# Kernel optimization log

Measured on AMD Instinct MI355X. Metric: run time of the kernel, lower is better.

## Reference

```python
import jax, jax.numpy as jnp
import numpy as np


def setup_inputs() -> dict:
    key = jax.random.key(0)
    ks = jax.random.split(key, 6)
    dim, dt_rank, dim_inner, d_state, channels, batch = 1024, 64, 1024, 128, 64, 8
    rn = lambda k, shape, sc: (jax.random.normal(k, shape, jnp.float32) * sc)
    return {
        "x": rn(ks[0], (batch, channels, dim), 1.0),
        "proj_w": rn(ks[1], (dim, dim), dim ** -0.5),
        "proj_b": jnp.zeros((dim,), jnp.float32),
        "conv_w": rn(ks[2], (channels, channels, 3), (channels * 3) ** -0.5),
        "conv_b": jnp.zeros((channels,), jnp.float32),
        "deltaBC_w": rn(ks[3], (dt_rank + 2 * d_state, dim), dim ** -0.5),
        "dt_proj_w": rn(ks[4], (dim_inner, dt_rank), dt_rank ** -0.5),
        "dt_proj_b": jnp.zeros((dim_inner,), jnp.float32),
        "A_log": jnp.log(jnp.broadcast_to(
            jnp.arange(1, d_state + 1, dtype=jnp.float32), (dim_inner, d_state))),
        "D": jnp.ones((dim_inner,), jnp.float32),
    }


def _silu(x):
    return x * jax.nn.sigmoid(x)


def _selective_scan(x, delta, A, B, C, D):
    # x, delta: (b, l, ed); A: (ed, n); B, C: (b, l, n); D: (ed)
    deltaA = jnp.exp(delta[..., None] * A)                      # (b, l, ed, n)
    BX = delta[..., None] * B[:, :, None, :] * x[..., None]     # (b, l, ed, n)

    def binop(e1, e2):
        a1, b1 = e1
        a2, b2 = e2
        return a1 * a2, a2 * b1 + b2

    # h_t = deltaA_t * h_{t-1} + BX_t  (parallel scan over sequence axis)
    _, hs = jax.lax.associative_scan(binop, (deltaA, BX), axis=1)
    y = jnp.einsum("blen,bln->ble", hs, C) + D * x
    return y


def reference(x, proj_w, proj_b, conv_w, conv_b, deltaBC_w,
              dt_proj_w, dt_proj_b, A_log, D):
    dt_rank = dt_proj_w.shape[1]
    d_state = A_log.shape[1]

    skip = x
    # same self.proj applied to both branches
    x1 = x @ proj_w.T + proj_b
    x2 = x1

    # Conv1d over the feature axis, treating seq positions as channels (L == channels)
    x1 = jax.lax.conv_general_dilated(
        x1, conv_w, window_strides=(1,), padding=[(1, 1)],
        dimension_numbers=("NCH", "OIH", "NCH")) + conv_b[None, :, None]
    x1 = _silu(x1)

    # SSM
    A = -jnp.exp(A_log)
    dbc = x1 @ deltaBC_w.T                                      # (b, l, dt_rank + 2n)
    delta = dbc[..., :dt_rank]
    Bm = dbc[..., dt_rank:dt_rank + d_state]
    Cm = dbc[..., dt_rank + d_state:]
    delta = jax.nn.softplus(delta @ dt_proj_w.T + dt_proj_b)    # (b, l, ed)
    y = _selective_scan(x1, delta, A, Bm, Cm, D)

    out = y * _silu(x2) + skip
    return out @ proj_w.T + proj_b
```

## Files before the change

kernel.cpp:

```cpp
#include <hip/hip_runtime.h>
#include <hip/hip_bf16.h>
#include <math.h>

typedef __hip_bfloat16 bf16;
typedef __attribute__((ext_vector_type(8))) short bf16x8;
typedef __attribute__((ext_vector_type(4))) float f32x4;

#define DIM     1024
#define DT_RANK 64
#define D_STATE 128
#define CHAN    64
#define BATCH   8
#define ROWS    (BATCH*CHAN)
#define DBC_N   (DT_RANK + 2*D_STATE)

#define SZ_X    (ROWS*DIM)
#define SZ_PW   (DIM*DIM)
#define SZ_PB   (DIM)
#define SZ_CW   (CHAN*CHAN*3)
#define SZ_CB   (CHAN)
#define SZ_DBCW (DBC_N*DIM)
#define SZ_DTW  (DIM*DT_RANK)
#define SZ_DTB  (DIM)
#define SZ_ALOG (DIM*D_STATE)
#define SZ_D    (DIM)

#define O0 0
#define O1 (O0+SZ_X)
#define O2 (O1+SZ_PW)
#define O3 (O2+SZ_PB)
#define O4 (O3+SZ_CW)
#define O5 (O4+SZ_CB)
#define O6 (O5+SZ_DBCW)
#define O7 (O6+SZ_DTW)
#define O8 (O7+SZ_DTB)
#define O9 (O8+SZ_ALOG)
#define TOTAL (O9+SZ_D)

#define BF16_ONES_PAIR 0x3F803F80u

__device__ __forceinline__ unsigned short f2b(float v) {
    bf16 t = __float2bfloat16(v);
    return *reinterpret_cast<unsigned short*>(&t);
}
__device__ __forceinline__ float b162f(unsigned short s) {
    return __uint_as_float(((unsigned)s) << 16);
}
__device__ __forceinline__ const bf16* SELP(const void* din, const bf16* wsp, int isb) {
    return isb ? (const bf16*)din : wsp;
}

__global__ __launch_bounds__(256) void convert_kernel(
    const void* __restrict__ s0, const void* __restrict__ s1,
    const void* __restrict__ s2, const void* __restrict__ s3,
    const void* __restrict__ s4, const void* __restrict__ s5,
    const void* __restrict__ s6, const void* __restrict__ s7,
    const void* __restrict__ s8, const void* __restrict__ s9,
    bf16* __restrict__ dstb)
{
    if (*(const unsigned*)s9 == BF16_ONES_PAIR) return;
    int idx = (blockIdx.x * 256 + threadIdx.x) * 4;
    if (idx >= TOTAL) return;
    const void* src; int base;
    if      (idx < O1) { src = s0; base = O0; }
    else if (idx < O2) { src = s1; base = O1; }
    else if (idx < O3) { src = s2; base = O2; }
    else if (idx < O4) { src = s3; base = O3; }
    else if (idx < O5) { src = s4; base = O4; }
    else if (idx < O6) { src = s5; base = O5; }
    else if (idx < O7) { src = s6; base = O6; }
    else if (idx < O8) { src = s7; base = O7; }
    else if (idx < O9) { src = s8; base = O8; }
    else               { src = s9; base = O9; }
    const int rel = idx - base;
    float4 v = *reinterpret_cast<const float4*>((const float*)src + rel);
    ushort4 u; u.x = f2b(v.x); u.y = f2b(v.y); u.z = f2b(v.z); u.w = f2b(v.w);
    *reinterpret_cast<ushort4*>(&dstb[idx]) = u;
}

template<int ACT, int OUTMODE, int K>
__global__ __launch_bounds__(256) void gemm_mfma(
    const void* __restrict__ Ad, const bf16* __restrict__ Aw,
    const void* __restrict__ Bd, const bf16* __restrict__ Bw,
    const void* __restrict__ biasd, const bf16* __restrict__ biasw,
    void* __restrict__ C0, bf16* __restrict__ C1,
    int lda, int ldb, int ldc, const unsigned* __restrict__ dsrc)
{
    __shared__ float red[4][32][36];
    const int isb = (*dsrc == BF16_ONES_PAIR) ? 1 : 0;
    const bf16* A = SELP(Ad, Aw, isb);
    const bf16* B = SELP(Bd, Bw, isb);
    const bf16* bias = (Ad == nullptr && Aw == nullptr) ? nullptr : nullptr;
    const bf16* biasp = (biasd || biasw) ? SELP(biasd, biasw, isb) : nullptr;

    const int l  = threadIdx.x & 63;
    const int w  = threadIdx.x >> 6;
    const int m0 = blockIdx.y * 32;
    const int n0 = blockIdx.x * 32;
    const int fr = l & 15;
    const int ko = (l >> 4) * 8;
    (void)bias;

    const bf16* Abase = A + (size_t)(m0 + fr) * lda + ko;
    const bf16* Bbase = B + (size_t)(n0 + fr) * ldb + ko;

    f32x4 acc00 = {}, acc01 = {}, acc10 = {}, acc11 = {};

    #pragma unroll 4
    for (int ks = w; ks * 32 < K; ks += 4) {
        const int k0 = ks * 32;
        bf16x8 a0 = *reinterpret_cast<const bf16x8*>(Abase + k0);
        bf16x8 a1 = *reinterpret_cast<const bf16x8*>(Abase + (size_t)16 * lda + k0);
        bf16x8 b0 = *reinterpret_cast<const bf16x8*>(Bbase + k0);
        bf16x8 b1 = *reinterpret_cast<const bf16x8*>(Bbase + (size_t)16 * ldb + k0);
        acc00 = __builtin_amdgcn_mfma_f32_16x16x32_bf16(a0, b0, acc00, 0, 0, 0);
        acc01 = __builtin_amdgcn_mfma_f32_16x16x32_bf16(a0, b1, acc01, 0, 0, 0);
        acc10 = __builtin_amdgcn_mfma_f32_16x16x32_bf16(a1, b0, acc10, 0, 0, 0);
        acc11 = __builtin_amdgcn_mfma_f32_16x16x32_bf16(a1, b1, acc11, 0, 0, 0);
    }

    {
        const int cr = (l >> 4) * 4;
        const int cc = l & 15;
        #pragma unroll
        for (int v = 0; v < 4; ++v) {
            red[w][cr + v][cc]           = acc00[v];
            red[w][cr + v][16 + cc]      = acc01[v];
            red[w][16 + cr + v][cc]      = acc10[v];
            red[w][16 + cr + v][16 + cc] = acc11[v];
        }
    }
    __syncthreads();

    const int t = threadIdx.x;
    const int r = t >> 3;
    const int c = (t & 7) * 4;
    float o[4];
    #pragma unroll
    for (int q = 0; q < 4; ++q) {
        float s = red[0][r][c + q] + red[1][r][c + q]
                + red[2][r][c + q] + red[3][r][c + q];
        if (biasp) s += __bfloat162float(biasp[n0 + c + q]);
        if (ACT == 1) s = (s > 20.0f) ? s : log1pf(__expf(s));
        o[q] = s;
    }
    const int m = m0 + r, nn = n0 + c;
    const size_t off = (size_t)m * ldc + nn;
    if (OUTMODE == 0) {
        *reinterpret_cast<float4*>((float*)C0 + off) = make_float4(o[0], o[1], o[2], o[3]);
    } else if (OUTMODE == 3) {
        ushort4 u; u.x = f2b(o[0]); u.y = f2b(o[1]); u.z = f2b(o[2]); u.w = f2b(o[3]);
        *reinterpret_cast<ushort4*>(C1 + off) = u;
    } else {
        if (isb) {
            ushort4 u; u.x = f2b(o[0]); u.y = f2b(o[1]); u.z = f2b(o[2]); u.w = f2b(o[3]);
            *reinterpret_cast<ushort4*>((bf16*)C0 + off) = u;
        } else {
            *reinterpret_cast<float4*>((float*)C0 + off) = make_float4(o[0], o[1], o[2], o[3]);
        }
    }
}

__global__ __launch_bounds__(256) void conv_silu_kernel(
    const float* __restrict__ xin,
    const void* __restrict__ cwd, const bf16* __restrict__ cww,
    const void* __restrict__ cbd, const bf16* __restrict__ cbw,
    float* __restrict__ xout, bf16* __restrict__ xout_bf,
    const unsigned* __restrict__ dsrc)
{
    const int isb = (*dsrc == BF16_ONES_PAIR) ? 1 : 0;
    const bf16* cw = SELP(cwd, cww, isb);
    const bf16* cb = SELP(cbd, cbw, isb);
    const int n   = blockIdx.x & 7;
    const int o   = blockIdx.x >> 3;
    const int tid = threadIdx.x;
    const int h0  = tid * 4;
    const float* xrow = xin + (size_t)n * CHAN * DIM;
    const bf16* wrow = cw + o * CHAN * 3;
    float acc0 = 0.f, acc1 = 0.f, acc2 = 0.f, acc3 = 0.f;
    #pragma unroll 4
    for (int i = 0; i < CHAN; ++i) {
        const float* xr = xrow + (size_t)i * DIM;
        const float4 xv = *reinterpret_cast<const float4*>(&xr[h0]);
        const float left  = (h0 > 0)        ? xr[h0 - 1] : 0.0f;
        const float right = (h0 + 4 < DIM)  ? xr[h0 + 4] : 0.0f;
        const float w0 = __bfloat162float(wrow[i * 3 + 0]);
        const float w1 = __bfloat162float(wrow[i * 3 + 1]);
        const float w2 = __bfloat162float(wrow[i * 3 + 2]);
        acc0 = fmaf(left, w0, fmaf(xv.x, w1, fmaf(xv.y, w2, acc0)));
        acc1 = fmaf(xv.x, w0, fmaf(xv.y, w1, fmaf(xv.z, w2, acc1)));
        acc2 = fmaf(xv.y, w0, fmaf(xv.z, w1, fmaf(xv.w, w2, acc2)));
        acc3 = fmaf(xv.z, w0, fmaf(xv.w, w1, fmaf(right, w2, acc3)));
    }
    const float bb = __bfloat162float(cb[o]);
    size_t base = (size_t)(n * CHAN + o) * DIM + h0;
    float v0 = acc0 + bb, v1 = acc1 + bb, v2 = acc2 + bb, v3 = acc3 + bb;
    v0 = v0 / (1.0f + __expf(-v0));
    v1 = v1 / (1.0f + __expf(-v1));
    v2 = v2 / (1.0f + __expf(-v2));
    v3 = v3 / (1.0f + __expf(-v3));
    *reinterpret_cast<float4*>(&xout[base]) = make_float4(v0, v1, v2, v3);
    ushort4 u; u.x = f2b(v0); u.y = f2b(v1); u.z = f2b(v2); u.w = f2b(v3);
    *reinterpret_cast<ushort4*>(&xout_bf[base]) = u;
}

__device__ __forceinline__ float sum8_dpp(float x) {
    int v;
    v = __builtin_amdgcn_update_dpp(0, __float_as_int(x), 0x111, 0xf, 0xf, true); x += __int_as_float(v);
    v = __builtin_amdgcn_update_dpp(0, __float_as_int(x), 0x112, 0xf, 0xf, true); x += __int_as_float(v);
    v = __builtin_amdgcn_update_dpp(0, __float_as_int(x), 0x114, 0xf, 0xf, true); x += __int_as_float(v);
    return x;
}

__global__ __launch_bounds__(512) void scan_kernel(
    const void* __restrict__ xd,  const bf16* __restrict__ xw,
    const float* __restrict__ x2,
    const float* __restrict__ xc,
    const bf16*  __restrict__ dbc_bf,
    const void* __restrict__ dtwd, const bf16* __restrict__ dtww,
    const void* __restrict__ dtbd, const bf16* __restrict__ dtbw,
    const void* __restrict__ alogd, const bf16* __restrict__ alogw,
    const void* __restrict__ dvd,  const bf16* __restrict__ dvw,
    bf16*        __restrict__ outp)
{
    __shared__ unsigned short sBC[CHAN][264];
    __shared__ float2 sPart[CHAN][8][8];
    __shared__ float sDB[CHAN][16][2];
    __shared__ float sPxc[CHAN][16];
    const int isb = (*(const unsigned*)dvd == BF16_ONES_PAIR) ? 1 : 0;
    const bf16* x_bf = SELP(xd, xw, isb);
    const bf16* dtw  = SELP(dtwd, dtww, isb);
    const bf16* dtb  = SELP(dtbd, dtbw, isb);
    const bf16* alog = SELP(alogd, alogw, isb);
    const bf16* dvec = SELP(dvd, dvw, isb);

    const int tid  = threadIdx.x;
    const int w    = tid >> 6;
    const int lane = tid & 63;
    const int bb   = blockIdx.x & 7;
    const int eb0  = (blockIdx.x >> 3) * 16;
    const int r0   = bb * CHAN;

    const int e0 = eb0 + 2 * w;
    const float C_LOG2E = 1.44269504f;
    const ushort2 alu0 = *reinterpret_cast<const ushort2*>(
        (const unsigned short*)alog + (size_t)e0 * D_STATE + 2 * lane);
    const ushort2 alu1 = *reinterpret_cast<const ushort2*>(
        (const unsigned short*)alog + (size_t)(e0 + 1) * D_STATE + 2 * lane);
    const float a00 = -__expf(b162f(alu0.x)) * C_LOG2E;
    const float a01 = -__expf(b162f(alu0.y)) * C_LOG2E;
    const float a10 = -__expf(b162f(alu1.x)) * C_LOG2E;
    const float a11 = -__expf(b162f(alu1.y)) * C_LOG2E;

    f32x4 acc = {};
    if (w < 4) {
        const int fr = lane & 15;
        const int ko = (lane >> 4) * 8;
        const bf16* Ab = dbc_bf + (size_t)(r0 + 16 * w + fr) * DBC_N + ko;
        const bf16* Bb = dtw + (size_t)(eb0 + fr) * DT_RANK + ko;
        bf16x8 fa0 = *reinterpret_cast<const bf16x8*>(Ab);
        bf16x8 fa1 = *reinterpret_cast<const bf16x8*>(Ab + 32);
        bf16x8 fb0 = *reinterpret_cast<const bf16x8*>(Bb);
        bf16x8 fb1 = *reinterpret_cast<const bf16x8*>(Bb + 32);
        acc = __builtin_amdgcn_mfma_f32_16x16x32_bf16(fa0, fb0, acc, 0, 0, 0);
        acc = __builtin_amdgcn_mfma_f32_16x16x32_bf16(fa1, fb1, acc, 0, 0, 0);
    } else {
        const int t2 = tid - 256;
        {
            const int row = t2 >> 2, q = t2 & 3;
            const uint4* src = reinterpret_cast<const uint4*>(
                dbc_bf + (size_t)(r0 + row) * DBC_N + DT_RANK + q * 64);
            uint4* dst = reinterpret_cast<uint4*>(&sBC[row][q * 64]);
            #pragma unroll
            for (int k = 0; k < 8; ++k) dst[k] = src[k];
        }
        {
            const int row = t2 >> 2, j = (t2 & 3) * 4;
            const float4 pc = *reinterpret_cast<const float4*>(
                &xc[(size_t)(r0 + row) * DIM + eb0 + j]);
            *reinterpret_cast<float4*>(&sPxc[row][j]) = pc;
        }
    }
    __syncthreads();

    if (w < 4) {
        const int cr = (lane >> 4) * 4, cc = lane & 15;
        const float bia = __bfloat162float(dtb[eb0 + cc]);
        #pragma unroll
        for (int v = 0; v < 4; ++v) {
            const int row = 16 * w + cr + v;
            float pre = acc[v] + bia;
            float dlt = (pre > 20.0f) ? pre : log1pf(__expf(pre));
            sDB[row][cc][0] = dlt;
            sDB[row][cc][1] = dlt * sPxc[row][cc];
        }
    }
    __syncthreads();

    float h00 = 0.f, h01 = 0.f, h10 = 0.f, h11 = 0.f;
    unsigned bu = *reinterpret_cast<const unsigned*>(&sBC[0][2 * lane]);
    unsigned cu = *reinterpret_cast<const unsigned*>(&sBC[0][128 + 2 * lane]);
    float4 db = *reinterpret_cast<const float4*>(&sDB[0][2 * w][0]);

    #pragma unroll 8
    for (int l = 0; l < CHAN; ++l) {
        const int ln = (l + 1) & 63;
        const unsigned bun = *reinterpret_cast<const unsigned*>(&sBC[ln][2 * lane]);
        const unsigned cun = *reinterpret_cast<const unsigned*>(&sBC[ln][128 + 2 * lane]);
        const float4 dbn = *reinterpret_cast<const float4*>(&sDB[ln][2 * w][0]);

        const float bv0 = __uint_as_float(bu << 16);
        const float bv1 = __uint_as_float(bu & 0xffff0000u);
        const float cv0 = __uint_as_float(cu << 16);
        const float cv1 = __uint_as_float(cu & 0xffff0000u);

        const float e00 = exp2f(db.x * a00);
        const float e01 = exp2f(db.x * a01);
        h00 = fmaf(e00, h00, db.y * bv0);
        h01 = fmaf(e01, h01, db.y * bv1);
        const float p0 = sum8_dpp(fmaf(h00, cv0, h01 * cv1));

        const float e10 = exp2f(db.z * a10);
        const float e11 = exp2f(db.z * a11);
        h10 = fmaf(e10, h10, db.w * bv0);
        h11 = fmaf(e11, h11, db.w * bv1);
        const float p1 = sum8_dpp(fmaf(h10, cv0, h11 * cv1));

        if ((lane & 7) == 7)
            sPart[l][lane >> 3][w] = make_float2(p0, p1);

        bu = bun; cu = cun; db = dbn;
    }
    __syncthreads();

    {
        const int le = tid >> 3;
        const int wp = tid & 7;
        float y0 = 0.f, y1 = 0.f;
        #pragma unroll
        for (int q = 0; q < 8; ++q) {
            const float2 p = sPart[le][q][wp];
            y0 += p.x; y1 += p.y;
        }
        const int e = eb0 + 2 * wp;
        const size_t off = (size_t)(r0 + le) * DIM + e;
        const float  xv0 = sPxc[le][2 * wp], xv1 = sPxc[le][2 * wp + 1];
        const float2 x2v = *reinterpret_cast<const float2*>(&x2[off]);
        const ushort2 xs = *reinterpret_cast<const ushort2*>(
            (const unsigned short*)x_bf + off);
        const ushort2 dv = *reinterpret_cast<const ushort2*>(
            (const unsigned short*)dvec + e);
        const float ga0 = x2v.x / (1.0f + __expf(-x2v.x));
        const float ga1 = x2v.y / (1.0f + __expf(-x2v.y));
        ushort2 u;
        u.x = f2b(fmaf(y0 + b162f(dv.x) * xv0, ga0, b162f(xs.x)));
        u.y = f2b(fmaf(y1 + b162f(dv.y) * xv1, ga1, b162f(xs.y)));
        *reinterpret_cast<ushort2*>(&outp[off]) = u;
    }
}

extern "C" void kernel_launch(void* const* d_in, const int* in_sizes, int n_in,
                              void* d_out, int out_size, void* d_ws, size_t ws_size,
                              hipStream_t stream) {
    bf16* inB = (bf16*)d_ws;
    float* x1_pre  = (float*)(inB + TOTAL);
    float* x1c     = x1_pre + (size_t)ROWS * DIM;
    bf16*  x1c_bf  = (bf16*)(x1c + (size_t)ROWS * DIM);
    bf16*  dbc_bf  = x1c_bf + (size_t)ROWS * DIM;
    bf16*  outp_bf = dbc_bf + (size_t)ROWS * DBC_N;
    const unsigned* dsrc = (const unsigned*)d_in[9];

    convert_kernel<<<(TOTAL / 4 + 255) / 256, 256, 0, stream>>>(
        d_in[0], d_in[1], d_in[2], d_in[3], d_in[4],
        d_in[5], d_in[6], d_in[7], d_in[8], d_in[9], inB);

    gemm_mfma<0, 0, DIM><<<dim3(DIM / 32, ROWS / 32), 256, 0, stream>>>(
        d_in[0], inB + O0, d_in[1], inB + O1, d_in[2], inB + O2,
        x1_pre, nullptr, DIM, DIM, DIM, dsrc);
    conv_silu_kernel<<<dim3(CHAN * BATCH), 256, 0, stream>>>(
        x1_pre, d_in[3], inB + O3, d_in[4], inB + O4, x1c, x1c_bf, dsrc);
    gemm_mfma<0, 3, DIM><<<dim3(DBC_N / 32, ROWS / 32), 256, 0, stream>>>(
        nullptr, x1c_bf, d_in[5], inB + O5, nullptr, nullptr,
        nullptr, dbc_bf, DIM, DIM, DBC_N, dsrc);
    scan_kernel<<<dim3(BATCH * (DIM / 16)), 512, 0, stream>>>(
        d_in[0], inB + O0, x1_pre, x1c, dbc_bf,
        d_in[6], inB + O6, d_in[7], inB + O7, d_in[8], inB + O8,
        d_in[9], inB + O9, outp_bf);
    gemm_mfma<0, 1, DIM><<<dim3(DIM / 32, ROWS / 32), 256, 0, stream>>>(
        nullptr, outp_bf, d_in[1], inB + O1, d_in[2], inB + O2,
        d_out, nullptr, DIM, DIM, DIM, dsrc);
}
```

Baseline: 96.87 us.

## Replace split-K 32x32 GEMM tiles with 64x64 tiles, one quadrant per wave

Each block now covers a 64x64 output tile, with every wave computing a 32x32 quadrant over the full K range. This replaces the earlier split-K layout where four waves shared one 32x32 tile and reduced their partial sums through shared memory. The change removes the LDS reduction and the barrier, and bias and softplus are applied straight from the accumulators. In exchange there are 4x fewer blocks (128 for the main GEMMs and only 40 for the deltaBC GEMM), each wave runs a K loop four times longer, and outputs are written as scalar strided stores instead of vector stores.

```diff
diff --git a/kernel.cpp b/kernel.cpp
--- a/kernel.cpp
+++ b/kernel.cpp
@@ -79,27 +79,26 @@
 }
 
 template<int ACT, int OUTMODE, int K>
-__global__ __launch_bounds__(256) void gemm_mfma(
+__global__ __launch_bounds__(256) void gemm64(
     const void* __restrict__ Ad, const bf16* __restrict__ Aw,
     const void* __restrict__ Bd, const bf16* __restrict__ Bw,
     const void* __restrict__ biasd, const bf16* __restrict__ biasw,
     void* __restrict__ C0, bf16* __restrict__ C1,
     int lda, int ldb, int ldc, const unsigned* __restrict__ dsrc)
 {
-    __shared__ float red[4][32][36];
     const int isb = (*dsrc == BF16_ONES_PAIR) ? 1 : 0;
     const bf16* A = SELP(Ad, Aw, isb);
     const bf16* B = SELP(Bd, Bw, isb);
-    const bf16* bias = (Ad == nullptr && Aw == nullptr) ? nullptr : nullptr;
     const bf16* biasp = (biasd || biasw) ? SELP(biasd, biasw, isb) : nullptr;
 
-    const int l  = threadIdx.x & 63;
-    const int w  = threadIdx.x >> 6;
-    const int m0 = blockIdx.y * 32;
-    const int n0 = blockIdx.x * 32;
-    const int fr = l & 15;
-    const int ko = (l >> 4) * 8;
-    (void)bias;
+    const int lane = threadIdx.x & 63;
+    const int w    = threadIdx.x >> 6;
+    const int qm   = (w >> 1) * 32;
+    const int qn   = (w & 1) * 32;
+    const int m0   = blockIdx.y * 64 + qm;
+    const int n0   = blockIdx.x * 64 + qn;
+    const int fr   = lane & 15;
+    const int ko   = (lane >> 4) * 8;
 
     const bf16* Abase = A + (size_t)(m0 + fr) * lda + ko;
     const bf16* Bbase = B + (size_t)(n0 + fr) * ldb + ko;
@@ -107,8 +106,7 @@
     f32x4 acc00 = {}, acc01 = {}, acc10 = {}, acc11 = {};
 
     #pragma unroll 4
-    for (int ks = w; ks * 32 < K; ks += 4) {
-        const int k0 = ks * 32;
+    for (int k0 = 0; k0 < K; k0 += 32) {
         bf16x8 a0 = *reinterpret_cast<const bf16x8*>(Abase + k0);
         bf16x8 a1 = *reinterpret_cast<const bf16x8*>(Abase + (size_t)16 * lda + k0);
         bf16x8 b0 = *reinterpret_cast<const bf16x8*>(Bbase + k0);
@@ -119,44 +117,45 @@
         acc11 = __builtin_amdgcn_mfma_f32_16x16x32_bf16(a1, b1, acc11, 0, 0, 0);
     }
 
-    {
-        const int cr = (l >> 4) * 4;
-        const int cc = l & 15;
-        #pragma unroll
-        for (int v = 0; v < 4; ++v) {
-            red[w][cr + v][cc]           = acc00[v];
-            red[w][cr + v][16 + cc]      = acc01[v];
-            red[w][16 + cr + v][cc]      = acc10[v];
-            red[w][16 + cr + v][16 + cc] = acc11[v];
-        }
-    }
-    __syncthreads();
-
-    const int t = threadIdx.x;
-    const int r = t >> 3;
-    const int c = (t & 7) * 4;
-    float o[4];
+    const int cr = (lane >> 4) * 4;
+    const int cc = lane & 15;
+    const float bias0 = biasp ? __bfloat162float(biasp[n0 + cc])      : 0.0f;
+    const float bias1 = biasp ? __bfloat162float(biasp[n0 + 16 + cc]) : 0.0f;
+
     #pragma unroll
-    for (int q = 0; q < 4; ++q) {
-        float s = red[0][r][c + q] + red[1][r][c + q]
-                + red[2][r][c + q] + red[3][r][c + q];
-        if (biasp) s += __bfloat162float(biasp[n0 + c + q]);
-        if (ACT == 1) s = (s > 20.0f) ? s : log1pf(__expf(s));
-        o[q] = s;
-    }
-    const int m = m0 + r, nn = n0 + c;
-    const size_t off = (size_t)m * ldc + nn;
-    if (OUTMODE == 0) {
-        *reinterpret_cast<float4*>((float*)C0 + off) = make_float4(o[0], o[1], o[2], o[3]);
-    } else if (OUTMODE == 3) {
-        ushort4 u; u.x = f2b(o[0]); u.y = f2b(o[1]); u.z = f2b(o[2]); u.w = f2b(o[3]);
-        *reinterpret_cast<ushort4*>(C1 + off) = u;
-    } else {
-        if (isb) {
-            ushort4 u; u.x = f2b(o[0]); u.y = f2b(o[1]); u.z = f2b(o[2]); u.w = f2b(o[3]);
-            *reinterpret_cast<ushort4*>((bf16*)C0 + off) = u;
+    for (int v = 0; v < 4; ++v) {
+        const int row0 = m0 + cr + v;
+        const int row1 = row0 + 16;
+        float o00 = acc00[v] + bias0;
+        float o01 = acc01[v] + bias1;
+        float o10 = acc10[v] + bias0;
+        float o11 = acc11[v] + bias1;
+        if (ACT == 1) {
+            o00 = (o00 > 20.0f) ? o00 : log1pf(__expf(o00));
+            o01 = (o01 > 20.0f) ? o01 : log1pf(__expf(o01));
+            o10 = (o10 > 20.0f) ? o10 : log1pf(__expf(o10));
+            o11 = (o11 > 20.0f) ? o11 : log1pf(__expf(o11));
+        }
+        const size_t off00 = (size_t)row0 * ldc + n0 + cc;
+        const size_t off01 = off00 + 16;
+        const size_t off10 = (size_t)row1 * ldc + n0 + cc;
+        const size_t off11 = off10 + 16;
+        if (OUTMODE == 0) {
+            ((float*)C0)[off00] = o00; ((float*)C0)[off01] = o01;
+            ((float*)C0)[off10] = o10; ((float*)C0)[off11] = o11;
+        } else if (OUTMODE == 3) {
+            C1[off00] = __float2bfloat16(o00); C1[off01] = __float2bfloat16(o01);
+            C1[off10] = __float2bfloat16(o10); C1[off11] = __float2bfloat16(o11);
         } else {
-            *reinterpret_cast<float4*>((float*)C0 + off) = make_float4(o[0], o[1], o[2], o[3]);
+            if (isb) {
+                ((bf16*)C0)[off00] = __float2bfloat16(o00);
+                ((bf16*)C0)[off01] = __float2bfloat16(o01);
+                ((bf16*)C0)[off10] = __float2bfloat16(o10);
+                ((bf16*)C0)[off11] = __float2bfloat16(o11);
+            } else {
+                ((float*)C0)[off00] = o00; ((float*)C0)[off01] = o01;
+                ((float*)C0)[off10] = o10; ((float*)C0)[off11] = o11;
+            }
         }
     }
 }
@@ -374,19 +373,19 @@
         d_in[0], d_in[1], d_in[2], d_in[3], d_in[4],
         d_in[5], d_in[6], d_in[7], d_in[8], d_in[9], inB);
 
-    gemm_mfma<0, 0, DIM><<<dim3(DIM / 32, ROWS / 32), 256, 0, stream>>>(
+    gemm64<0, 0, DIM><<<dim3(DIM / 64, ROWS / 64), 256, 0, stream>>>(
         d_in[0], inB + O0, d_in[1], inB + O1, d_in[2], inB + O2,
         x1_pre, nullptr, DIM, DIM, DIM, dsrc);
     conv_silu_kernel<<<dim3(CHAN * BATCH), 256, 0, stream>>>(
         x1_pre, d_in[3], inB + O3, d_in[4], inB + O4, x1c, x1c_bf, dsrc);
-    gemm_mfma<0, 3, DIM><<<dim3(DBC_N / 32, ROWS / 32), 256, 0, stream>>>(
+    gemm64<0, 3, DIM><<<dim3(DBC_N / 64, ROWS / 64), 256, 0, stream>>>(
         nullptr, x1c_bf, d_in[5], inB + O5, nullptr, nullptr,
         nullptr, dbc_bf, DIM, DIM, DBC_N, dsrc);
     scan_kernel<<<dim3(BATCH * (DIM / 16)), 512, 0, stream>>>(
         d_in[0], inB + O0, x1_pre, x1c, dbc_bf,
         d_in[6], inB + O6, d_in[7], inB + O7, d_in[8], inB + O8,
         d_in[9], inB + O9, outp_bf);
-    gemm_mfma<0, 1, DIM><<<dim3(DIM / 32, ROWS / 32), 256, 0, stream>>>(
+    gemm64<0, 1, DIM><<<dim3(DIM / 64, ROWS / 64), 256, 0, stream>>>(
         nullptr, outp_bf, d_in[1], inB + O1, d_in[2], inB + O2,
         d_out, nullptr, DIM, DIM, DIM, dsrc);
 }
```

Result: slower. 124.9 us (+28.9%).
